# Kernel optimization log

Hardware: AMD Instinct MI355X
Metric: run time of the kernel (lower is better)

The kernel has to match this reference:

```python
import jax, jax.numpy as jnp
import numpy as np

N = 98304   # nodes
E = 393216  # directed edges (avg degree 4)
B = 4096    # graphs


def setup_inputs() -> dict:
    key = jax.random.key(0)
    ks = iter(jax.random.split(key, 40))
    rn = lambda shape, s=0.05: jax.random.normal(next(ks), shape, jnp.float32) * s
    inp = {
        'x': jax.random.normal(next(ks), (N, 78), jnp.float32),
        'edge_index': jax.random.randint(next(ks), (2, E), 0, N, jnp.int32),
        # sorted graph assignment covering all B graphs (~24 nodes each)
        'batch': ((jnp.arange(N, dtype=jnp.int32) * B) // N).astype(jnp.int32),
        'target': jax.random.normal(next(ks), (B, 800), jnp.float32),
        'fingerprint': jax.random.normal(next(ks), (B, 167), jnp.float32),
        # GCN layers (PyG GCNConv: transform then sym-normalized aggregate)
        'W1': rn((78, 78)), 'b1': jnp.zeros((78,), jnp.float32),
        'W2': rn((78, 156)), 'b2': jnp.zeros((156,), jnp.float32),
        'W3': rn((156, 312)), 'b3': jnp.zeros((312,), jnp.float32),
        'Wg1': rn((312, 1024)), 'bg1': jnp.zeros((1024,), jnp.float32),
        'Wg2': rn((1024, 128)), 'bg2': jnp.zeros((128,), jnp.float32),
        'Wd': rn((800, 512)), 'bd': jnp.zeros((512,), jnp.float32),
        'Wd2': rn((512, 256)), 'bd2': jnp.zeros((256,), jnp.float32),
        'Wd3': rn((256, 128)), 'bd3': jnp.zeros((128,), jnp.float32),
        'Wfp': rn((167, 128)), 'bfp': jnp.zeros((128,), jnp.float32),
        'Wf1': rn((256, 1024)), 'bf1': jnp.zeros((1024,), jnp.float32),
        'Wf2': rn((1024, 512)), 'bf2': jnp.zeros((512,), jnp.float32),
        'Wo': rn((512, 1)), 'bo': jnp.zeros((1,), jnp.float32),
    }
    return inp


def reference(x, edge_index, batch, target, fingerprint,
              W1, b1, W2, b2, W3, b3, Wg1, bg1, Wg2, bg2,
              Wd, bd, Wd2, bd2, Wd3, bd3, Wfp, bfp,
              Wf1, bf1, Wf2, bf2, Wo, bo):
    src, dst = edge_index[0], edge_index[1]
    loop = jnp.arange(N, dtype=src.dtype)
    s = jnp.concatenate([src, loop])  # with self-loops
    d = jnp.concatenate([dst, loop])
    deg = jax.ops.segment_sum(jnp.ones(s.shape[0], jnp.float32), d, num_segments=N)
    dinv = jnp.where(deg > 0, jax.lax.rsqrt(deg), 0.0)
    norm = (dinv[s] * dinv[d])[:, None]  # [E+N, 1]

    def gcn(h, W, b):
        h = h @ W  # transform first (PyG GCNConv)
        msg = h[s] * norm  # gather + scale
        return jax.ops.segment_sum(msg, d, num_segments=N) + b

    h = jax.nn.relu(gcn(x, W1, b1))
    h = jax.nn.relu(gcn(h, W2, b2))
    h = jax.nn.relu(gcn(h, W3, b3))
    g = jax.ops.segment_max(h, batch, num_segments=B)  # global max pool [B, 312]
    g = jax.nn.relu(g @ Wg1 + bg1)
    g = g @ Wg2 + bg2  # dropout is identity in eval

    xt = jax.nn.relu(target @ Wd + bd)
    xt = jax.nn.relu(xt @ Wd2 + bd2)
    xt = xt @ Wd3 + bd3

    fp = fingerprint @ Wfp + bfp  # computed but unused, faithful to source
    del fp

    xc = jnp.concatenate([g, xt], axis=1)  # [B, 256]
    xc = jax.nn.relu(xc @ Wf1 + bf1)
    xc = jax.nn.relu(xc @ Wf2 + bf2)
    return xc @ Wo + bo  # [B, 1]
```

## Files before the change

### kernel.cpp

```cpp
#include <hip/hip_runtime.h>

static constexpr int NNODE = 98304;
static constexpr int NEDGE = 393216;
static constexpr int NB    = 4096;
static constexpr int CAP   = 32;

typedef __attribute__((ext_vector_type(8))) short  short8;
typedef __attribute__((ext_vector_type(8))) unsigned short ushort8;
typedef __attribute__((ext_vector_type(4))) float  f32x4;

__device__ inline unsigned short f2bf(float x) {
    unsigned int u = __float_as_uint(x);
    u += 0x7fffu + ((u >> 16) & 1u);
    return (unsigned short)(u >> 16);
}
__device__ inline float bf2f(unsigned short h) {
    return __uint_as_float(((unsigned int)h) << 16);
}

static constexpr int OW1 = 0,         NW1 = 78 * 96;
static constexpr int OW2 = OW1 + NW1, NW2 = 156 * 96;
static constexpr int OW3 = OW2 + NW2, NW3 = 312 * 160;
static constexpr int OG1 = OW3 + NW3, NG1 = 1024 * 320;
static constexpr int OG2 = OG1 + NG1, NG2 = 128 * 1024;
static constexpr int OD1 = OG2 + NG2, ND1 = 512 * 800;
static constexpr int OD2 = OD1 + ND1, ND2 = 256 * 512;
static constexpr int OD3 = OD2 + ND2, ND3 = 128 * 256;
static constexpr int OF1 = OD3 + ND3, NF1 = 1024 * 256;
static constexpr int OF2 = OF1 + NF1, NF2 = 512 * 1024;
static constexpr int WTOT = OF2 + NF2;


__global__ void k_zeroi(int* p, int n) {
    int i = blockIdx.x * blockDim.x + threadIdx.x;
    if (i < n) p[i] = 0;
}

__global__ void k_fillv(float* p, float v, int n) {
    int i = blockIdx.x * blockDim.x + threadIdx.x;
    if (i < n) p[i] = v;
}

__global__ void k_counti(const int* __restrict__ dst, int* cnt, int e) {
    int i = blockIdx.x * blockDim.x + threadIdx.x;
    if (i < e) atomicAdd(&cnt[dst[i]], 1);
}

__global__ void k_dinv(const int* __restrict__ cnt, float* dinv, int n) {
    int i = blockIdx.x * blockDim.x + threadIdx.x;
    if (i < n) dinv[i] = rsqrtf(1.0f + (float)cnt[i]);
}

__global__ void k_bucket(const int* __restrict__ src, const int* __restrict__ dst,
                         const float* __restrict__ dinv, int* pos,
                         int* __restrict__ bsrc, float* __restrict__ bnrm, int e) {
    int i = blockIdx.x * blockDim.x + threadIdx.x;
    if (i >= e) return;
    int s = src[i], d = dst[i];
    int p = atomicAdd(&pos[d], 1);
    if (p < CAP) {
        bsrc[(size_t)d * CAP + p] = s;
        bnrm[(size_t)d * CAP + p] = dinv[s] * dinv[d];
    }
}

__global__ void k_sortbk(const int* __restrict__ cnt, int* __restrict__ bsrc,
                         float* __restrict__ bnrm, int n) {
    int node = blockIdx.x * blockDim.x + threadIdx.x;
    if (node >= n) return;
    int deg = min(cnt[node], CAP);
    size_t base = (size_t)node * CAP;
    for (int i = 1; i < deg; ++i) {
        int s = bsrc[base + i];
        float v = bnrm[base + i];
        int j = i - 1;
        while (j >= 0 && bsrc[base + j] > s) {
            bsrc[base + j + 1] = bsrc[base + j];
            bnrm[base + j + 1] = bnrm[base + j];
            --j;
        }
        bsrc[base + j + 1] = s;
        bnrm[base + j + 1] = v;
    }
}

struct SJob  { const float* src; int K, N, K32, off; };
struct SJobs { SJob j[10]; };

__global__ void k_splitw(SJobs js, unsigned short* __restrict__ WH,
                         unsigned short* __restrict__ WL) {
    int tid = blockIdx.x * blockDim.x + threadIdx.x;
    int stride = gridDim.x * blockDim.x;
    #pragma unroll 1
    for (int w = 0; w < 10; ++w) {
        SJob jb = js.j[w];
        int tot = jb.N * jb.K32;
        for (int i = tid; i < tot; i += stride) {
            int n = i / jb.K32, k = i - n * jb.K32;
            float x = (k < jb.K) ? jb.src[(size_t)k * jb.N + n] : 0.0f;
            unsigned short h = f2bf(x);
            WH[jb.off + i] = h;
            WL[jb.off + i] = f2bf(x - bf2f(h));
        }
    }
}

template<int DIM, int KS>
__global__ void k_gather_sp(const float* __restrict__ t, const int* __restrict__ cnt,
                            const int* __restrict__ bsrc, const float* __restrict__ bnrm,
                            const float* __restrict__ dinv,
                            unsigned short* __restrict__ Ph,
                            unsigned short* __restrict__ Pl, int n) {
    constexpr int H = KS / 2;
    int i = blockIdx.x * blockDim.x + threadIdx.x;
    if (i >= n * H) return;
    int node = i / H;
    int c2 = (i - node * H) * 2;
    size_t o = (size_t)node * KS + c2;
    if (c2 >= DIM) {
        *(unsigned int*)&Ph[o] = 0u;
        *(unsigned int*)&Pl[o] = 0u;
        return;
    }
    float di = dinv[node];
    float2 tv = *(const float2*)&t[(size_t)node * DIM + c2];
    float sx = tv.x * di * di, sy = tv.y * di * di;
    int deg = min(cnt[node], CAP);
    size_t base = (size_t)node * CAP;
    for (int j = 0; j < deg; ++j) {
        int s = bsrc[base + j];
        float nrm = bnrm[base + j];
        float2 v = *(const float2*)&t[(size_t)s * DIM + c2];
        sx += v.x * nrm;
        sy += v.y * nrm;
    }
    unsigned short hx = f2bf(sx), hy = f2bf(sy);
    unsigned short lx = f2bf(sx - bf2f(hx)), ly = f2bf(sy - bf2f(hy));
    *(unsigned int*)&Ph[o] = (unsigned int)hx | ((unsigned int)hy << 16);
    *(unsigned int*)&Pl[o] = (unsigned int)lx | ((unsigned int)ly << 16);
}

template<bool HAS_BIAS, bool RELU, bool POOL, bool ASPLIT>
__global__ __launch_bounds__(256)
void k_gemm_mf(const float* __restrict__ A,
               const unsigned short* __restrict__ Ahg, const unsigned short* __restrict__ Alg,
               const unsigned short* __restrict__ Wth, const unsigned short* __restrict__ Wtl,
               const float* __restrict__ bias, const int* __restrict__ batch,
               float* __restrict__ C, int M, int N, int K, int Kb, int ldc) {
    __shared__ __align__(16) unsigned char smraw[20480];
    ushort (*Ah)[40] = (ushort(*)[40])(smraw);
    ushort (*Al)[40] = (ushort(*)[40])(smraw + 5120);
    ushort (*Bh)[40] = (ushort(*)[40])(smraw + 10240);
    ushort (*Bl)[40] = (ushort(*)[40])(smraw + 15360);
    __shared__ int sb[64];

    const int tid  = threadIdx.x;
    const int lane = tid & 63;
    const int wv = tid >> 6, wr = wv >> 1, wc = wv & 1;
    const int m16 = lane & 15, kg = lane >> 4;
    const int row0 = blockIdx.y * 64, col0 = blockIdx.x * 64;
    const int mA = tid >> 2, kqA = (tid & 3) << 3;

    if (POOL && tid < 64) sb[tid] = batch[row0 + tid];

    f32x4 acc[2][2];
    #pragma unroll
    for (int i = 0; i < 2; ++i)
        #pragma unroll
        for (int j = 0; j < 2; ++j)
            acc[i][j] = f32x4{0.f, 0.f, 0.f, 0.f};

    for (int k0 = 0; k0 < Kb; k0 += 32) {
        if (ASPLIT) {
            size_t ao = (size_t)(row0 + mA) * Kb + k0 + kqA;
            *(ushort8*)&Ah[mA][kqA] = *(const ushort8*)&Ahg[ao];
            *(ushort8*)&Al[mA][kqA] = *(const ushort8*)&Alg[ao];
        } else {
            int gr = row0 + mA;
            const float* ap = A + (size_t)gr * K + k0 + kqA;
            ushort8 vh, vl;
            #pragma unroll
            for (int u = 0; u < 8; ++u) {
                float xv = (gr < M && (k0 + kqA + u) < K) ? ap[u] : 0.f;
                unsigned short h = f2bf(xv);
                vh[u] = h; vl[u] = f2bf(xv - bf2f(h));
            }
            *(ushort8*)&Ah[mA][kqA] = vh;
            *(ushort8*)&Al[mA][kqA] = vl;
        }
        {
            int gn = col0 + mA;
            if (gn < N) {
                size_t bo = (size_t)gn * Kb + k0 + kqA;
                *(ushort8*)&Bh[mA][kqA] = *(const ushort8*)&Wth[bo];
                *(ushort8*)&Bl[mA][kqA] = *(const ushort8*)&Wtl[bo];
            } else {
                ushort8 z = {0, 0, 0, 0, 0, 0, 0, 0};
                *(ushort8*)&Bh[mA][kqA] = z;
                *(ushort8*)&Bl[mA][kqA] = z;
            }
        }
        __syncthreads();

        short8 ah[2], al[2], bh[2], bl[2];
        #pragma unroll
        for (int i = 0; i < 2; ++i) {
            ah[i] = *(const short8*)&Ah[wr * 32 + i * 16 + m16][kg * 8];
            al[i] = *(const short8*)&Al[wr * 32 + i * 16 + m16][kg * 8];
            bh[i] = *(const short8*)&Bh[wc * 32 + i * 16 + m16][kg * 8];
            bl[i] = *(const short8*)&Bl[wc * 32 + i * 16 + m16][kg * 8];
        }
        #pragma unroll
        for (int i = 0; i < 2; ++i)
            #pragma unroll
            for (int j = 0; j < 2; ++j) {
                acc[i][j] = __builtin_amdgcn_mfma_f32_16x16x32_bf16(ah[i], bh[j], acc[i][j], 0, 0, 0);
                acc[i][j] = __builtin_amdgcn_mfma_f32_16x16x32_bf16(ah[i], bl[j], acc[i][j], 0, 0, 0);
                acc[i][j] = __builtin_amdgcn_mfma_f32_16x16x32_bf16(al[i], bh[j], acc[i][j], 0, 0, 0);
            }
        __syncthreads();
    }

    if (!POOL) {
        #pragma unroll
        for (int i = 0; i < 2; ++i)
            #pragma unroll
            for (int r = 0; r < 4; ++r) {
                int gr = row0 + wr * 32 + i * 16 + kg * 4 + r;
                if (gr >= M) continue;
                #pragma unroll
                for (int j = 0; j < 2; ++j) {
                    int gn = col0 + wc * 32 + j * 16 + m16;
                    if (gn >= N) continue;
                    float v = acc[i][j][r];
                    if (HAS_BIAS) v += bias[gn];
                    if (RELU) v = fmaxf(v, 0.0f);
                    C[(size_t)gr * ldc + gn] = v;
                }
            }
    } else {
        float (*Ts)[68] = (float(*)[68])smraw;
        #pragma unroll
        for (int i = 0; i < 2; ++i)
            #pragma unroll
            for (int r = 0; r < 4; ++r) {
                int lr = wr * 32 + i * 16 + kg * 4 + r;
                #pragma unroll
                for (int j = 0; j < 2; ++j) {
                    int lc = wc * 32 + j * 16 + m16;
                    int gn = col0 + lc;
                    float bv = (gn < N) ? bias[gn] : 0.0f;
                    Ts[lr][lc] = fmaxf(acc[i][j][r] + bv, 0.0f);
                }
            }
        __syncthreads();
        int seg = tid >> 6, col = tid & 63;
        int gcol = col0 + col;
        if (gcol < N) {
            int gb = sb[0] + seg;
            float mx = -1.0f;
            for (int r = 0; r < 64; ++r)
                if (sb[r] == gb) mx = fmaxf(mx, Ts[r][col]);
            if (mx >= 0.0f)
                atomicMax((int*)&C[(size_t)gb * N + gcol], __float_as_int(mx));
        }
    }
}

__global__ __launch_bounds__(256)
void k_rowdot(const float* __restrict__ A, const float* __restrict__ w,
              const float* __restrict__ b, float* __restrict__ out, int M, int K) {
    int wave = (blockIdx.x * blockDim.x + threadIdx.x) >> 6;
    int lane = threadIdx.x & 63;
    if (wave >= M) return;
    const float* row = A + (size_t)wave * K;
    float s = 0.0f;
    for (int k = lane; k < K; k += 64) s += row[k] * w[k];
    #pragma unroll
    for (int off = 32; off > 0; off >>= 1) s += __shfl_down(s, off, 64);
    if (lane == 0) out[wave] = s + b[0];
}


extern "C" void kernel_launch(void* const* d_in, const int* in_sizes, int n_in,
                              void* d_out, int out_size, void* d_ws, size_t ws_size,
                              hipStream_t stream) {
    const float* x      = (const float*)d_in[0];
    const int*   ei     = (const int*)d_in[1];
    const int*   batch  = (const int*)d_in[2];
    const float* target = (const float*)d_in[3];
    const float* W1  = (const float*)d_in[5],  *b1  = (const float*)d_in[6];
    const float* W2  = (const float*)d_in[7],  *b2  = (const float*)d_in[8];
    const float* W3  = (const float*)d_in[9],  *b3  = (const float*)d_in[10];
    const float* Wg1 = (const float*)d_in[11], *bg1 = (const float*)d_in[12];
    const float* Wg2 = (const float*)d_in[13], *bg2 = (const float*)d_in[14];
    const float* Wd  = (const float*)d_in[15], *bd  = (const float*)d_in[16];
    const float* Wd2 = (const float*)d_in[17], *bd2 = (const float*)d_in[18];
    const float* Wd3 = (const float*)d_in[19], *bd3 = (const float*)d_in[20];
    const float* Wf1 = (const float*)d_in[23], *bf1 = (const float*)d_in[24];
    const float* Wf2 = (const float*)d_in[25], *bf2 = (const float*)d_in[26];
    const float* Wo  = (const float*)d_in[27], *bo  = (const float*)d_in[28];
    float* out = (float*)d_out;

    const int* src = ei;
    const int* dst = ei + NEDGE;

    char* pb = (char*)d_ws;
    auto alloc = [&](size_t bytes) { char* r = pb; pb += (bytes + 255) & ~(size_t)255; return r; };
    float* dinv = (float*)alloc((size_t)NNODE * 4);
    int*   cnt  = (int*)  alloc((size_t)NNODE * 4);
    int*   pos  = (int*)  alloc((size_t)NNODE * 4);
    int*   bsrc = (int*)  alloc((size_t)NNODE * CAP * 4);
    float* bnrm = (float*)alloc((size_t)NNODE * CAP * 4);
    unsigned short* WH = (unsigned short*)alloc((size_t)WTOT * 2);
    unsigned short* WL = (unsigned short*)alloc((size_t)WTOT * 2);
    unsigned short* Ph = (unsigned short*)alloc((size_t)NNODE * 160 * 2);
    unsigned short* Pl = (unsigned short*)alloc((size_t)NNODE * 160 * 2);
    float* Q = (float*)alloc((size_t)NNODE * 156 * 4);

    float* gpool = Q;
    float* g1    = gpool + (size_t)NB * 312;
    float* xc    = g1    + (size_t)NB * 1024;
    float* xt1   = xc    + (size_t)NB * 256;
    float* xt2   = xt1   + (size_t)NB * 512;
    float* xc1   = (float*)Ph;
    float* xc2   = xc1   + (size_t)NB * 1024;

    SJobs js = {{
        { W1,   78,   78,   96,  OW1 },
        { W2,   78,  156,   96,  OW2 },
        { W3,  156,  312,  160,  OW3 },
        { Wg1, 312, 1024,  320,  OG1 },
        { Wg2, 1024, 128, 1024,  OG2 },
        { Wd,  800,  512,  800,  OD1 },
        { Wd2, 512,  256,  512,  OD2 },
        { Wd3, 256,  128,  256,  OD3 },
        { Wf1, 256, 1024,  256,  OF1 },
        { Wf2, 1024, 512, 1024,  OF2 },
    }};
    k_splitw<<<512, 256, 0, stream>>>(js, WH, WL);

    k_zeroi <<<(2 * NNODE + 255) / 256, 256, 0, stream>>>(cnt, 2 * NNODE);
    k_counti<<<(NEDGE + 255) / 256, 256, 0, stream>>>(dst, cnt, NEDGE);
    k_dinv  <<<(NNODE + 255) / 256, 256, 0, stream>>>(cnt, dinv, NNODE);
    k_bucket<<<(NEDGE + 255) / 256, 256, 0, stream>>>(src, dst, dinv, pos, bsrc, bnrm, NEDGE);
    k_sortbk<<<(NNODE + 255) / 256, 256, 0, stream>>>(cnt, bsrc, bnrm, NNODE);

    k_gather_sp<78, 96><<<(NNODE * 48 + 255) / 256, 256, 0, stream>>>(x, cnt, bsrc, bnrm, dinv, Ph, Pl, NNODE);
    k_gemm_mf<true, true, false, true><<<dim3(2, NNODE / 64), 256, 0, stream>>>(
        nullptr, Ph, Pl, WH + OW1, WL + OW1, b1, nullptr, Q, NNODE, 78, 96, 96, 78);

    k_gather_sp<78, 96><<<(NNODE * 48 + 255) / 256, 256, 0, stream>>>(Q, cnt, bsrc, bnrm, dinv, Ph, Pl, NNODE);
    k_gemm_mf<true, true, false, true><<<dim3(3, NNODE / 64), 256, 0, stream>>>(
        nullptr, Ph, Pl, WH + OW2, WL + OW2, b2, nullptr, Q, NNODE, 156, 96, 96, 156);

    k_gather_sp<156, 160><<<(NNODE * 80 + 255) / 256, 256, 0, stream>>>(Q, cnt, bsrc, bnrm, dinv, Ph, Pl, NNODE);
    k_fillv<<<((NB * 312) + 255) / 256, 256, 0, stream>>>(gpool, 0.0f, NB * 312);
    k_gemm_mf<true, true, true, true><<<dim3(5, NNODE / 64), 256, 0, stream>>>(
        nullptr, Ph, Pl, WH + OW3, WL + OW3, b3, batch, gpool, NNODE, 312, 160, 160, 312);

    k_gemm_mf<true, true,  false, false><<<dim3(16, NB / 64), 256, 0, stream>>>(
        gpool, nullptr, nullptr, WH + OG1, WL + OG1, bg1, nullptr, g1, NB, 1024, 312, 320, 1024);
    k_gemm_mf<true, false, false, false><<<dim3(2, NB / 64), 256, 0, stream>>>(
        g1, nullptr, nullptr, WH + OG2, WL + OG2, bg2, nullptr, xc, NB, 128, 1024, 1024, 256);

    k_gemm_mf<true, true,  false, false><<<dim3(8, NB / 64), 256, 0, stream>>>(
        target, nullptr, nullptr, WH + OD1, WL + OD1, bd, nullptr, xt1, NB, 512, 800, 800, 512);
    k_gemm_mf<true, true,  false, false><<<dim3(4, NB / 64), 256, 0, stream>>>(
        xt1, nullptr, nullptr, WH + OD2, WL + OD2, bd2, nullptr, xt2, NB, 256, 512, 512, 256);
    k_gemm_mf<true, false, false, false><<<dim3(2, NB / 64), 256, 0, stream>>>(
        xt2, nullptr, nullptr, WH + OD3, WL + OD3, bd3, nullptr, xc + 128, NB, 128, 256, 256, 256);

    k_gemm_mf<true, true, false, false><<<dim3(16, NB / 64), 256, 0, stream>>>(
        xc, nullptr, nullptr, WH + OF1, WL + OF1, bf1, nullptr, xc1, NB, 1024, 256, 256, 1024);
    k_gemm_mf<true, true, false, false><<<dim3(8, NB / 64), 256, 0, stream>>>(
        xc1, nullptr, nullptr, WH + OF2, WL + OF2, bf2, nullptr, xc2, NB, 512, 1024, 1024, 512);

    k_rowdot<<<(NB * 64) / 256, 256, 0, stream>>>(xc2, Wo, bo, out, NB, 512);
}
```

Measured before the change: 900.1 us.

## Keep A tile resident across all output columns in GCN GEMMs; pre-split head activations

The GCN transform GEMMs now use one block per 64-row tile that loops over every output column tile (NT tiles), so each split-bf16 A tile is loaded once instead of once per column block. Weight buffers are padded to multiples of 64 columns so the B loads need no bounds checks. The MLP head GEMMs now write their outputs as pre-split bf16 high/low pairs, so the next GEMM can read them directly instead of re-splitting fp32 inputs. The cost is more shared memory and accumulator registers per block for the node GEMMs, which may lower occupancy, and the grid for those GEMMs shrinks.

Result: no change. 912.9 us (+1.4%).

```diff
diff --git a/kernel.cpp b/kernel.cpp
--- a/kernel.cpp
+++ b/kernel.cpp
@@ -18,9 +18,9 @@
     return __uint_as_float(((unsigned int)h) << 16);
 }
 
-static constexpr int OW1 = 0,         NW1 = 78 * 96;
-static constexpr int OW2 = OW1 + NW1, NW2 = 156 * 96;
-static constexpr int OW3 = OW2 + NW2, NW3 = 312 * 160;
+static constexpr int OW1 = 0,         NW1 = 128 * 96;
+static constexpr int OW2 = OW1 + NW1, NW2 = 192 * 96;
+static constexpr int OW3 = OW2 + NW2, NW3 = 320 * 160;
 static constexpr int OG1 = OW3 + NW3, NG1 = 1024 * 320;
 static constexpr int OG2 = OG1 + NG1, NG2 = 128 * 1024;
 static constexpr int OD1 = OG2 + NG2, ND1 = 512 * 800;
@@ -35,22 +35,18 @@
     int i = blockIdx.x * blockDim.x + threadIdx.x;
     if (i < n) p[i] = 0;
 }
-
 __global__ void k_fillv(float* p, float v, int n) {
     int i = blockIdx.x * blockDim.x + threadIdx.x;
     if (i < n) p[i] = v;
 }
-
 __global__ void k_counti(const int* __restrict__ dst, int* cnt, int e) {
     int i = blockIdx.x * blockDim.x + threadIdx.x;
     if (i < e) atomicAdd(&cnt[dst[i]], 1);
 }
-
 __global__ void k_dinv(const int* __restrict__ cnt, float* dinv, int n) {
     int i = blockIdx.x * blockDim.x + threadIdx.x;
     if (i < n) dinv[i] = rsqrtf(1.0f + (float)cnt[i]);
 }
-
 __global__ void k_bucket(const int* __restrict__ src, const int* __restrict__ dst,
                          const float* __restrict__ dinv, int* pos,
                          int* __restrict__ bsrc, float* __restrict__ bnrm, int e) {
@@ -63,7 +59,6 @@
         bnrm[(size_t)d * CAP + p] = dinv[s] * dinv[d];
     }
 }
-
 __global__ void k_sortbk(const int* __restrict__ cnt, int* __restrict__ bsrc,
                          float* __restrict__ bnrm, int n) {
     int node = blockIdx.x * blockDim.x + threadIdx.x;
@@ -84,7 +79,7 @@
     }
 }
 
-struct SJob  { const float* src; int K, N, K32, off; };
+struct SJob  { const float* src; int K, N, Npad, K32, off; };
 struct SJobs { SJob j[10]; };
 
 __global__ void k_splitw(SJobs js, unsigned short* __restrict__ WH,
@@ -94,10 +89,10 @@
     #pragma unroll 1
     for (int w = 0; w < 10; ++w) {
         SJob jb = js.j[w];
-        int tot = jb.N * jb.K32;
+        int tot = jb.Npad * jb.K32;
         for (int i = tid; i < tot; i += stride) {
             int n = i / jb.K32, k = i - n * jb.K32;
-            float x = (k < jb.K) ? jb.src[(size_t)k * jb.N + n] : 0.0f;
+            float x = (k < jb.K && n < jb.N) ? jb.src[(size_t)k * jb.N + n] : 0.0f;
             unsigned short h = f2bf(x);
             WH[jb.off + i] = h;
             WL[jb.off + i] = f2bf(x - bf2f(h));
@@ -140,19 +135,141 @@
     *(unsigned int*)&Pl[o] = (unsigned int)lx | ((unsigned int)ly << 16);
 }
 
-template<bool HAS_BIAS, bool RELU, bool POOL, bool ASPLIT>
+template<int NT, bool POOL>
 __global__ __launch_bounds__(256)
-void k_gemm_mf(const float* __restrict__ A,
-               const unsigned short* __restrict__ Ahg, const unsigned short* __restrict__ Alg,
-               const unsigned short* __restrict__ Wth, const unsigned short* __restrict__ Wtl,
-               const float* __restrict__ bias, const int* __restrict__ batch,
-               float* __restrict__ C, int M, int N, int K, int Kb, int ldc) {
+void k_gemm_nres(const unsigned short* __restrict__ Ahg, const unsigned short* __restrict__ Alg,
+                 const unsigned short* __restrict__ Wth, const unsigned short* __restrict__ Wtl,
+                 const float* __restrict__ bias, const int* __restrict__ batch,
+                 float* __restrict__ C, int M, int N, int Kb, int ldc) {
+    __shared__ __align__(16) unsigned char smraw[(1 + NT) * 10240];
+    ushort (*Ah)[40] = (ushort(*)[40])(smraw);
+    ushort (*Al)[40] = (ushort(*)[40])(smraw + 5120);
+    ushort (*Bh)[40] = (ushort(*)[40])(smraw + 10240);
+    ushort (*Bl)[40] = (ushort(*)[40])(smraw + 10240 + NT * 5120);
+    __shared__ int sb[64];
+
+    const int tid  = threadIdx.x;
+    const int lane = tid & 63;
+    const int wv = tid >> 6, wr = wv >> 1, wc = wv & 1;
+    const int m16 = lane & 15, kg = lane >> 4;
+    const int row0 = blockIdx.x * 64;
+    const int mA = tid >> 2, kqA = (tid & 3) << 3;
+
+    if (POOL && tid < 64) sb[tid] = batch[row0 + tid];
+
+    f32x4 acc[NT][2][2];
+    #pragma unroll
+    for (int ct = 0; ct < NT; ++ct)
+        #pragma unroll
+        for (int i = 0; i < 2; ++i)
+            #pragma unroll
+            for (int j = 0; j < 2; ++j)
+                acc[ct][i][j] = f32x4{0.f, 0.f, 0.f, 0.f};
+
+    for (int k0 = 0; k0 < Kb; k0 += 32) {
+        {
+            size_t ao = (size_t)(row0 + mA) * Kb + k0 + kqA;
+            *(ushort8*)&Ah[mA][kqA] = *(const ushort8*)&Ahg[ao];
+            *(ushort8*)&Al[mA][kqA] = *(const ushort8*)&Alg[ao];
+        }
+        #pragma unroll
+        for (int rep = 0; rep < NT; ++rep) {
+            int c = rep * 64 + mA;
+            size_t bo = (size_t)c * Kb + k0 + kqA;
+            *(ushort8*)&Bh[c][kqA] = *(const ushort8*)&Wth[bo];
+            *(ushort8*)&Bl[c][kqA] = *(const ushort8*)&Wtl[bo];
+        }
+        __syncthreads();
+
+        short8 ah[2], al[2];
+        #pragma unroll
+        for (int i = 0; i < 2; ++i) {
+            ah[i] = *(const short8*)&Ah[wr * 32 + i * 16 + m16][kg * 8];
+            al[i] = *(const short8*)&Al[wr * 32 + i * 16 + m16][kg * 8];
+        }
+        #pragma unroll
+        for (int ct = 0; ct < NT; ++ct) {
+            short8 bh[2], bl[2];
+            #pragma unroll
+            for (int j = 0; j < 2; ++j) {
+                bh[j] = *(const short8*)&Bh[ct * 64 + wc * 32 + j * 16 + m16][kg * 8];
+                bl[j] = *(const short8*)&Bl[ct * 64 + wc * 32 + j * 16 + m16][kg * 8];
+            }
+            #pragma unroll
+            for (int i = 0; i < 2; ++i)
+                #pragma unroll
+                for (int j = 0; j < 2; ++j) {
+                    acc[ct][i][j] = __builtin_amdgcn_mfma_f32_16x16x32_bf16(ah[i], bh[j], acc[ct][i][j], 0, 0, 0);
+                    acc[ct][i][j] = __builtin_amdgcn_mfma_f32_16x16x32_bf16(ah[i], bl[j], acc[ct][i][j], 0, 0, 0);
+                    acc[ct][i][j] = __builtin_amdgcn_mfma_f32_16x16x32_bf16(al[i], bh[j], acc[ct][i][j], 0, 0, 0);
+                }
+        }
+        __syncthreads();
+    }
+
+    if (!POOL) {
+        #pragma unroll
+        for (int ct = 0; ct < NT; ++ct)
+            #pragma unroll
+            for (int i = 0; i < 2; ++i)
+                #pragma unroll
+                for (int r = 0; r < 4; ++r) {
+                    int gr = row0 + wr * 32 + i * 16 + kg * 4 + r;
+                    #pragma unroll
+                    for (int j = 0; j < 2; ++j) {
+                        int gn = ct * 64 + wc * 32 + j * 16 + m16;
+                        if (gn < N) {
+                            float v = fmaxf(acc[ct][i][j][r] + bias[gn], 0.0f);
+                            C[(size_t)gr * ldc + gn] = v;
+                        }
+                    }
+                }
+    } else {
+        float (*Ts)[68] = (float(*)[68])smraw;
+        #pragma unroll 1
+        for (int ct = 0; ct < NT; ++ct) {
+            __syncthreads();
+            #pragma unroll
+            for (int i = 0; i < 2; ++i)
+                #pragma unroll
+                for (int r = 0; r < 4; ++r) {
+                    int lr = wr * 32 + i * 16 + kg * 4 + r;
+                    #pragma unroll
+                    for (int j = 0; j < 2; ++j) {
+                        int lc = wc * 32 + j * 16 + m16;
+                        int gn = ct * 64 + lc;
+                        float bv = (gn < N) ? bias[gn] : 0.0f;
+                        Ts[lr][lc] = fmaxf(acc[ct][i][j][r] + bv, 0.0f);
+                    }
+                }
+            __syncthreads();
+            int seg = tid >> 6, col = tid & 63;
+            int gcol = ct * 64 + col;
+            if (gcol < N) {
+                int gb = sb[0] + seg;
+                float mx = -1.0f;
+                for (int r = 0; r < 64; ++r)
+                    if (sb[r] == gb) mx = fmaxf(mx, Ts[r][col]);
+                if (mx >= 0.0f)
+                    atomicMax((int*)&C[(size_t)gb * N + gcol], __float_as_int(mx));
+            }
+        }
+    }
+}
+
+template<bool HAS_BIAS, bool RELU, bool ASPLIT, bool OSPLIT>
+__global__ __launch_bounds__(256)
+void k_gemm_head(const float* __restrict__ A,
+                 const unsigned short* __restrict__ Ahg, const unsigned short* __restrict__ Alg,
+                 const unsigned short* __restrict__ Wth, const unsigned short* __restrict__ Wtl,
+                 const float* __restrict__ bias, float* __restrict__ C,
+                 unsigned short* __restrict__ CH, unsigned short* __restrict__ CL,
+                 int M, int N, int K, int Kb, int ldc) {
     __shared__ __align__(16) unsigned char smraw[20480];
     ushort (*Ah)[40] = (ushort(*)[40])(smraw);
     ushort (*Al)[40] = (ushort(*)[40])(smraw + 5120);
     ushort (*Bh)[40] = (ushort(*)[40])(smraw + 10240);
     ushort (*Bl)[40] = (ushort(*)[40])(smraw + 15360);
-    __shared__ int sb[64];
 
     const int tid  = threadIdx.x;
     const int lane = tid & 63;
@@ -160,8 +277,6 @@
     const int m16 = lane & 15, kg = lane >> 4;
     const int row0 = blockIdx.y * 64, col0 = blockIdx.x * 64;
     const int mA = tid >> 2, kqA = (tid & 3) << 3;
-
-    if (POOL && tid < 64) sb[tid] = batch[row0 + tid];
 
     f32x4 acc[2][2];
     #pragma unroll
@@ -221,50 +336,28 @@
         __syncthreads();
     }
 
-    if (!POOL) {
-        #pragma unroll
-        for (int i = 0; i < 2; ++i)
-            #pragma unroll
-            for (int r = 0; r < 4; ++r) {
-                int gr = row0 + wr * 32 + i * 16 + kg * 4 + r;
-                if (gr >= M) continue;
-                #pragma unroll
-                for (int j = 0; j < 2; ++j) {
-                    int gn = col0 + wc * 32 + j * 16 + m16;
-                    if (gn >= N) continue;
-                    float v = acc[i][j][r];
-                    if (HAS_BIAS) v += bias[gn];
-                    if (RELU) v = fmaxf(v, 0.0f);
+    #pragma unroll
+    for (int i = 0; i < 2; ++i)
+        #pragma unroll
+        for (int r = 0; r < 4; ++r) {
+            int gr = row0 + wr * 32 + i * 16 + kg * 4 + r;
+            if (gr >= M) continue;
+            #pragma unroll
+            for (int j = 0; j < 2; ++j) {
+                int gn = col0 + wc * 32 + j * 16 + m16;
+                if (gn >= N) continue;
+                float v = acc[i][j][r];
+                if (HAS_BIAS) v += bias[gn];
+                if (RELU) v = fmaxf(v, 0.0f);
+                if (OSPLIT) {
+                    unsigned short h = f2bf(v);
+                    CH[(size_t)gr * ldc + gn] = h;
+                    CL[(size_t)gr * ldc + gn] = f2bf(v - bf2f(h));
+                } else {
                     C[(size_t)gr * ldc + gn] = v;
                 }
             }
-    } else {
-        float (*Ts)[68] = (float(*)[68])smraw;
-        #pragma unroll
-        for (int i = 0; i < 2; ++i)
-            #pragma unroll
-            for (int r = 0; r < 4; ++r) {
-                int lr = wr * 32 + i * 16 + kg * 4 + r;
-                #pragma unroll
-                for (int j = 0; j < 2; ++j) {
-                    int lc = wc * 32 + j * 16 + m16;
-                    int gn = col0 + lc;
-                    float bv = (gn < N) ? bias[gn] : 0.0f;
-                    Ts[lr][lc] = fmaxf(acc[i][j][r] + bv, 0.0f);
-                }
-            }
-        __syncthreads();
-        int seg = tid >> 6, col = tid & 63;
-        int gcol = col0 + col;
-        if (gcol < N) {
-            int gb = sb[0] + seg;
-            float mx = -1.0f;
-            for (int r = 0; r < 64; ++r)
-                if (sb[r] == gb) mx = fmaxf(mx, Ts[r][col]);
-            if (mx >= 0.0f)
-                atomicMax((int*)&C[(size_t)gb * N + gcol], __float_as_int(mx));
-        }
-    }
+        }
 }
 
 __global__ __launch_bounds__(256)
@@ -319,24 +412,29 @@
     float* Q = (float*)alloc((size_t)NNODE * 156 * 4);
 
     float* gpool = Q;
-    float* g1    = gpool + (size_t)NB * 312;
-    float* xc    = g1    + (size_t)NB * 1024;
-    float* xt1   = xc    + (size_t)NB * 256;
-    float* xt2   = xt1   + (size_t)NB * 512;
-    float* xc1   = (float*)Ph;
-    float* xc2   = xc1   + (size_t)NB * 1024;
+    unsigned short* g1H  = (unsigned short*)(gpool + (size_t)NB * 312);
+    unsigned short* g1L  = g1H  + (size_t)NB * 1024;
+    unsigned short* xcH  = g1L  + (size_t)NB * 1024;
+    unsigned short* xcL  = xcH  + (size_t)NB * 256;
+    unsigned short* xt1H = xcL  + (size_t)NB * 256;
+    unsigned short* xt1L = xt1H + (size_t)NB * 512;
+    unsigned short* xt2H = xt1L + (size_t)NB * 512;
+    unsigned short* xt2L = xt2H + (size_t)NB * 256;
+    unsigned short* xc1H = (unsigned short*)Ph;
+    unsigned short* xc1L = xc1H + (size_t)NB * 1024;
+    float* xc2 = (float*)(xc1L + (size_t)NB * 1024);
 
     SJobs js = {{
-        { W1,   78,   78,   96,  OW1 },
-        { W2,   78,  156,   96,  OW2 },
-        { W3,  156,  312,  160,  OW3 },
-        { Wg1, 312, 1024,  320,  OG1 },
-        { Wg2, 1024, 128, 1024,  OG2 },
-        { Wd,  800,  512,  800,  OD1 },
-        { Wd2, 512,  256,  512,  OD2 },
-        { Wd3, 256,  128,  256,  OD3 },
-        { Wf1, 256, 1024,  256,  OF1 },
-        { Wf2, 1024, 512, 1024,  OF2 },
+        { W1,   78,   78,  128,   96, OW1 },
+        { W2,   78,  156,  192,   96, OW2 },
+        { W3,  156,  312,  320,  160, OW3 },
+        { Wg1, 312, 1024, 1024,  320, OG1 },
+        { Wg2, 1024, 128,  128, 1024, OG2 },
+        { Wd,  800,  512,  512,  800, OD1 },
+        { Wd2, 512,  256,  256,  512, OD2 },
+        { Wd3, 256,  128,  128,  256, OD3 },
+        { Wf1, 256, 1024, 1024,  256, OF1 },
+        { Wf2, 1024, 512,  512, 1024, OF2 },
     }};
     k_splitw<<<512, 256, 0, stream>>>(js, WH, WL);
 
@@ -347,34 +445,31 @@
     k_sortbk<<<(NNODE + 255) / 256, 256, 0, stream>>>(cnt, bsrc, bnrm, NNODE);
 
     k_gather_sp<78, 96><<<(NNODE * 48 + 255) / 256, 256, 0, stream>>>(x, cnt, bsrc, bnrm, dinv, Ph, Pl, NNODE);
-    k_gemm_mf<true, true, false, true><<<dim3(2, NNODE / 64), 256, 0, stream>>>(
-        nullptr, Ph, Pl, WH + OW1, WL + OW1, b1, nullptr, Q, NNODE, 78, 96, 96, 78);
+    k_gemm_nres<2, false><<<NNODE / 64, 256, 0, stream>>>(Ph, Pl, WH + OW1, WL + OW1, b1, nullptr, Q, NNODE, 78, 96, 78);
 
     k_gather_sp<78, 96><<<(NNODE * 48 + 255) / 256, 256, 0, stream>>>(Q, cnt, bsrc, bnrm, dinv, Ph, Pl, NNODE);
-    k_gemm_mf<true, true, false, true><<<dim3(3, NNODE / 64), 256, 0, stream>>>(
-        nullptr, Ph, Pl, WH + OW2, WL + OW2, b2, nullptr, Q, NNODE, 156, 96, 96, 156);
+    k_gemm_nres<3, false><<<NNODE / 64, 256, 0, stream>>>(Ph, Pl, WH + OW2, WL + OW2, b2, nullptr, Q, NNODE, 156, 96, 156);
 
     k_gather_sp<156, 160><<<(NNODE * 80 + 255) / 256, 256, 0, stream>>>(Q, cnt, bsrc, bnrm, dinv, Ph, Pl, NNODE);
     k_fillv<<<((NB * 312) + 255) / 256, 256, 0, stream>>>(gpool, 0.0f, NB * 312);
-    k_gemm_mf<true, true, true, true><<<dim3(5, NNODE / 64), 256, 0, stream>>>(
-        nullptr, Ph, Pl, WH + OW3, WL + OW3, b3, batch, gpool, NNODE, 312, 160, 160, 312);
-
-    k_gemm_mf<true, true,  false, false><<<dim3(16, NB / 64), 256, 0, stream>>>(
-        gpool, nullptr, nullptr, WH + OG1, WL + OG1, bg1, nullptr, g1, NB, 1024, 312, 320, 1024);
-    k_gemm_mf<true, false, false, false><<<dim3(2, NB / 64), 256, 0, stream>>>(
-        g1, nullptr, nullptr, WH + OG2, WL + OG2, bg2, nullptr, xc, NB, 128, 1024, 1024, 256);
-
-    k_gemm_mf<true, true,  false, false><<<dim3(8, NB / 64), 256, 0, stream>>>(
-        target, nullptr, nullptr, WH + OD1, WL + OD1, bd, nullptr, xt1, NB, 512, 800, 800, 512);
-    k_gemm_mf<true, true,  false, false><<<dim3(4, NB / 64), 256, 0, stream>>>(
-        xt1, nullptr, nullptr, WH + OD2, WL + OD2, bd2, nullptr, xt2, NB, 256, 512, 512, 256);
-    k_gemm_mf<true, false, false, false><<<dim3(2, NB / 64), 256, 0, stream>>>(
-        xt2, nullptr, nullptr, WH + OD3, WL + OD3, bd3, nullptr, xc + 128, NB, 128, 256, 256, 256);
-
-    k_gemm_mf<true, true, false, false><<<dim3(16, NB / 64), 256, 0, stream>>>(
-        xc, nullptr, nullptr, WH + OF1, WL + OF1, bf1, nullptr, xc1, NB, 1024, 256, 256, 1024);
-    k_gemm_mf<true, true, false, false><<<dim3(8, NB / 64), 256, 0, stream>>>(
-        xc1, nullptr, nullptr, WH + OF2, WL + OF2, bf2, nullptr, xc2, NB, 512, 1024, 1024, 512);
+    k_gemm_nres<5, true><<<NNODE / 64, 256, 0, stream>>>(Ph, Pl, WH + OW3, WL + OW3, b3, batch, gpool, NNODE, 312, 160, 312);
+
+    k_gemm_head<true, true, false, true><<<dim3(16, NB / 64), 256, 0, stream>>>(
+        gpool, nullptr, nullptr, WH + OG1, WL + OG1, bg1, nullptr, g1H, g1L, NB, 1024, 312, 320, 1024);
+    k_gemm_head<true, false, true, true><<<dim3(2, NB / 64), 256, 0, stream>>>(
+        nullptr, g1H, g1L, WH + OG2, WL + OG2, bg2, nullptr, xcH, xcL, NB, 128, 1024, 1024, 256);
+
+    k_gemm_head<true, true, false, true><<<dim3(8, NB / 64), 256, 0, stream>>>(
+        target, nullptr, nullptr, WH + OD1, WL + OD1, bd, nullptr, xt1H, xt1L, NB, 512, 800, 800, 512);
+    k_gemm_head<true, true, true, true><<<dim3(4, NB / 64), 256, 0, stream>>>(
+        nullptr, xt1H, xt1L, WH + OD2, WL + OD2, bd2, nullptr, xt2H, xt2L, NB, 256, 512, 512, 256);
+    k_gemm_head<true, false, true, true><<<dim3(2, NB / 64), 256, 0, stream>>>(
+        nullptr, xt2H, xt2L, WH + OD3, WL + OD3, bd3, nullptr, xcH + 128, xcL + 128, NB, 128, 256, 256, 256);
+
+    k_gemm_head<true, true, true, true><<<dim3(16, NB / 64), 256, 0, stream>>>(
+        nullptr, xcH, xcL, WH + OF1, WL + OF1, bf1, nullptr, xc1H, xc1L, NB, 1024, 256, 256, 1024);
+    k_gemm_head<true, true, true, false><<<dim3(8, NB / 64), 256, 0, stream>>>(
+        nullptr, xc1H, xc1L, WH + OF2, WL + OF2, bf2, xc2, nullptr, nullptr, NB, 512, 1024, 1024, 512);
 
     k_rowdot<<<(NB * 64) / 256, 256, 0, stream>>>(xc2, Wo, bo, out, NB, 512);
 }
```
